# Kernel optimization log

Measured on AMD Instinct MI355X. Metric: run time of the kernel, lower is better.

Reference implementation:

```python
import jax, jax.numpy as jnp
import numpy as np

N_NODES = 100000


def gcn_conv(x, src, dst, deg_inv_sqrt, W, b):
    # x: [N, Fin], src/dst: [E_total] (self-loops included), W: [Fin, Fout]
    h = x @ W                                  # [N, Fout]
    norm = deg_inv_sqrt[src] * deg_inv_sqrt[dst]  # [E_total]
    msgs = h[src] * norm[:, None]              # [E_total, Fout] gather
    out = jax.ops.segment_sum(msgs, dst, num_segments=N_NODES)  # scatter-add
    return out + b


def setup_inputs() -> dict:
    key = jax.random.key(0)
    k1, k2, k3, k4, k5, k6, k7, k8 = jax.random.split(key, 8)
    input_dim, hidden_dim, out_dim = 4, 64, 2
    n_edges = 3200000
    x = jax.random.normal(k1, (N_NODES, input_dim), dtype=jnp.float32)
    edge_index = jax.random.randint(k2, (2, n_edges), 0, N_NODES, dtype=jnp.int64)
    s1 = 1.0 / np.sqrt(input_dim)
    s2 = 1.0 / np.sqrt(hidden_dim)
    W1 = jax.random.uniform(k3, (input_dim, hidden_dim), jnp.float32, -s1, s1)
    b1 = jnp.zeros((hidden_dim,), jnp.float32)
    W2 = jax.random.uniform(k4, (hidden_dim, hidden_dim), jnp.float32, -s2, s2)
    b2 = jnp.zeros((hidden_dim,), jnp.float32)
    Wf = jax.random.uniform(k5, (hidden_dim, out_dim), jnp.float32, -s2, s2)
    bf = jax.random.uniform(k6, (out_dim,), jnp.float32, -s2, s2)
    return {"x": x, "edge_index": edge_index, "W1": W1, "b1": b1,
            "W2": W2, "b2": b2, "Wf": Wf, "bf": bf}


def reference(x, edge_index, W1, b1, W2, b2, Wf, bf):
    # Add self-loops (PyG GCNConv default)
    loop = jnp.arange(N_NODES, dtype=edge_index.dtype)
    src = jnp.concatenate([edge_index[0], loop])
    dst = jnp.concatenate([edge_index[1], loop])
    # Symmetric normalization: degree on destination after self-loops
    deg = jax.ops.segment_sum(jnp.ones_like(dst, dtype=x.dtype), dst,
                              num_segments=N_NODES)
    deg_inv_sqrt = jnp.where(deg > 0, jax.lax.rsqrt(deg), 0.0)
    h = jax.nn.relu(gcn_conv(x, src, dst, deg_inv_sqrt, W1, b1))
    h = jax.nn.relu(gcn_conv(h, src, dst, deg_inv_sqrt, W2, b2))
    return h @ Wf + bf
```

## Files before the change

### kernel.cpp

```cpp
#include <hip/hip_runtime.h>
#include <hip/hip_bf16.h>

#define N_NODES 100000
#define N_EDGES 3200000
#define NB ((N_NODES + 255) / 256)
#define NBUCKET NB
#define EPB 8192
#define NPB ((N_EDGES + EPB - 1) / EPB)
#define BCAP 11264
#define KF_TILES (N_NODES / 16)
#define KF_BLOCKS ((KF_TILES + 3) / 4)
#define GCS 16
#define AGG_Q 4
#define AGG_QN (N_NODES / AGG_Q)

typedef short short8 __attribute__((ext_vector_type(8)));
typedef float f32x4 __attribute__((ext_vector_type(4)));

__device__ inline unsigned f2bf(float f) {
  unsigned x = __float_as_uint(f);
  return (x + 0x7FFFu + ((x >> 16) & 1u)) >> 16;
}


__global__ void __launch_bounds__(256) k_pass1(const int* __restrict__ src,
                                               const int* __restrict__ dst,
                                               int* __restrict__ gcur,
                                               unsigned int* __restrict__ eb) {
  __shared__ int hist[NBUCKET];
  __shared__ int gbase[NBUCKET];
  int tid = threadIdx.x;
  int base = blockIdx.x * EPB;
  int cnt = min(EPB, N_EDGES - base);
  int n4 = cnt >> 2;
  for (int i = tid; i < NBUCKET; i += 256) hist[i] = 0;
  __syncthreads();
  const int4* d4 = (const int4*)(dst + base);
  const int4* s4 = (const int4*)(src + base);
  unsigned mv[32];
  unsigned short mb[32];
#pragma unroll
  for (int k = 0; k < 8; ++k) {
    int i = tid + (k << 8);
    if (i < n4) {
      int4 dv = d4[i];
      int4 sv = s4[i];
      int b0 = dv.x >> 8, b1_ = dv.y >> 8, b2 = dv.z >> 8, b3 = dv.w >> 8;
      unsigned p0 = atomicAdd(&hist[b0], 1);
      unsigned p1 = atomicAdd(&hist[b1_], 1);
      unsigned p2 = atomicAdd(&hist[b2], 1);
      unsigned p3 = atomicAdd(&hist[b3], 1);
      mv[4 * k + 0] = (unsigned)sv.x | ((unsigned)(dv.x & 255) << 17) | (p0 << 25);
      mv[4 * k + 1] = (unsigned)sv.y | ((unsigned)(dv.y & 255) << 17) | (p1 << 25);
      mv[4 * k + 2] = (unsigned)sv.z | ((unsigned)(dv.z & 255) << 17) | (p2 << 25);
      mv[4 * k + 3] = (unsigned)sv.w | ((unsigned)(dv.w & 255) << 17) | (p3 << 25);
      mb[4 * k + 0] = (unsigned short)b0;
      mb[4 * k + 1] = (unsigned short)b1_;
      mb[4 * k + 2] = (unsigned short)b2;
      mb[4 * k + 3] = (unsigned short)b3;
    } else {
      mb[4 * k + 0] = 0xFFFF; mb[4 * k + 1] = 0xFFFF;
      mb[4 * k + 2] = 0xFFFF; mb[4 * k + 3] = 0xFFFF;
    }
  }
  __syncthreads();
  for (int b = tid; b < NBUCKET; b += 256) {
    int h = hist[b];
    gbase[b] = h ? atomicAdd(&gcur[b * GCS], h) : 0;
  }
  __syncthreads();
#pragma unroll
  for (int k = 0; k < 32; ++k) {
    if (mb[k] != 0xFFFF) {
      int b = mb[k];
      unsigned v = mv[k];
      unsigned pos = (unsigned)gbase[b] + (v >> 25);
      if (pos < BCAP) eb[(size_t)b * BCAP + pos] = v & 0x01FFFFFFu;
    }
  }
}


__global__ void __launch_bounds__(256) k_part2(unsigned int* __restrict__ eb,
                                               const int* __restrict__ gcur,
                                               int* __restrict__ rs, int* __restrict__ re,
                                               float* __restrict__ dis,
                                               const float4* __restrict__ x4,
                                               float4* __restrict__ xd) {
  __shared__ int hist[256], scn[256], cur[256];
  __shared__ int wsum[4];
  __shared__ int tot;
  __shared__ unsigned int stage[BCAP];
  int b = blockIdx.x, tid = threadIdx.x;
  int lane = tid & 63, wid = tid >> 6;
  int n0 = b << 8;
  int cnt = gcur[b * GCS];
  int base = b * BCAP;
  hist[tid] = 0; cur[tid] = 0;
  __syncthreads();
  for (int i = tid; i < cnt; i += 256)
    atomicAdd(&hist[eb[base + i] >> 17], 1);
  __syncthreads();
  int n = n0 + tid;
  int deg = hist[tid];
  int slots = (n < N_NODES) ? ((deg + 1 + 7) & ~7) : 0;
  int v = slots;
#pragma unroll
  for (int off = 1; off < 64; off <<= 1) {
    int t = __shfl_up(v, off);
    if (lane >= off) v += t;
  }
  if (lane == 63) wsum[wid] = v;
  __syncthreads();
  int x = v;
#pragma unroll
  for (int w2 = 0; w2 < 3; ++w2)
    if (wid > w2) x += wsum[w2];
  int excl = x - slots;
  if (tid == 255) tot = x;
  if (n < N_NODES) {
    rs[n]  = base + excl;
    re[n]  = base + excl + deg + 1;
    float dn = rsqrtf((float)(deg + 1));
    dis[n] = dn;
    float4 xv = x4[n];
    float4 w; w.x = xv.x * dn; w.y = xv.y * dn; w.z = xv.z * dn; w.w = xv.w * dn;
    xd[n] = w;
    stage[excl] = (unsigned)n;
    for (int i = deg + 1; i < slots; ++i)
      stage[excl + i] = (unsigned)N_NODES;
  }
  if (b == 0 && tid == 0) xd[N_NODES] = make_float4(0.f, 0.f, 0.f, 0.f);
  scn[tid] = excl + 1;
  __syncthreads();
  for (int i = tid; i < cnt; i += 256) {
    unsigned v2 = eb[base + i];
    unsigned low = v2 >> 17;
    int lpos = scn[low] + atomicAdd(&cur[low], 1);
    stage[lpos] = v2 & 0x1FFFFu;
  }
  __syncthreads();
  int total = tot;
  for (int i = tid; i < total; i += 256)
    eb[base + i] = stage[i];
  if (tid < 16) {
    int gp = total + tid;
    if (gp < BCAP) eb[base + gp] = (unsigned)N_NODES;
  }
}


__global__ void __launch_bounds__(256) k_l1(const float4* __restrict__ xd,
                                            const float* __restrict__ dis,
                                            const int* __restrict__ rs,
                                            const int* __restrict__ re,
                                            const int* __restrict__ csr,
                                            const float* __restrict__ W1,
                                            const float* __restrict__ b1,
                                            unsigned int* __restrict__ h1o) {
  int gt = blockIdx.x * 256 + threadIdx.x;
  int nid = gt >> 2, p = gt & 3;
  if (nid > N_NODES) return;
  if (nid == N_NODES) {
    uint4 z = make_uint4(0u, 0u, 0u, 0u);
    uint4* op = (uint4*)(h1o + nid * 32 + p * 8);
    op[0] = z; op[1] = z;
    return;
  }
  int e0 = rs[nid];
  int it4 = ((re[nid] - e0 + 7) & ~7) >> 2;
  const int* cp = csr + e0 + p;
  float ax = 0.f, ay = 0.f, az = 0.f, aw = 0.f;
#pragma unroll 4
  for (int t = 0; t < it4; ++t) {
    int s = cp[t << 2];
    float4 v = xd[s];
    ax += v.x; ay += v.y; az += v.z; aw += v.w;
  }
  ax += __shfl_xor(ax, 1); ax += __shfl_xor(ax, 2);
  ay += __shfl_xor(ay, 1); ay += __shfl_xor(ay, 2);
  az += __shfl_xor(az, 1); az += __shfl_xor(az, 2);
  aw += __shfl_xor(aw, 1); aw += __shfl_xor(aw, 2);
  float dn = dis[nid];
  ax *= dn; ay *= dn; az *= dn; aw *= dn;
  int j0 = p << 4;
  unsigned ou[8];
#pragma unroll
  for (int j2 = 0; j2 < 8; ++j2) {
    int j = j0 + j2 * 2;
    float s0 = b1[j]     + ax * W1[j]     + ay * W1[64 + j]     + az * W1[128 + j]     + aw * W1[192 + j];
    float s1 = b1[j + 1] + ax * W1[j + 1] + ay * W1[64 + j + 1] + az * W1[128 + j + 1] + aw * W1[192 + j + 1];
    unsigned u0 = f2bf(fmaxf(s0, 0.f) * dn);
    unsigned u1 = f2bf(fmaxf(s1, 0.f) * dn);
    ou[j2] = u0 | (u1 << 16);
  }
  uint4* op = (uint4*)(h1o + nid * 32 + p * 8);
  op[0] = make_uint4(ou[0], ou[1], ou[2], ou[3]);
  op[1] = make_uint4(ou[4], ou[5], ou[6], ou[7]);
}


__device__ inline void acc_bf2(float& a0, float& a1, unsigned u) {
  a0 += __uint_as_float(u << 16);
  a1 += __uint_as_float(u & 0xffff0000u);
}

__global__ void __launch_bounds__(256)
k_agg(const __hip_bfloat16* __restrict__ h1s, const float* __restrict__ dis,
      const int* __restrict__ rs, const int* __restrict__ re,
      const int* __restrict__ csr, unsigned short* __restrict__ aggb,
      int n_base) {
  int l = threadIdx.x & 63;
  int w = threadIdx.x >> 6;
  int n = n_base + blockIdx.x * 4 + w;
  int g = l >> 3;
  int c = l & 7;

  const unsigned int* h32 = (const unsigned int*)h1s;
  int e0 = rs[n];
  int iter = (re[n] - e0 + 7) >> 3;
  const int* cb = csr + e0 + g;
  int coff = c << 2;

  float a0 = 0.f, a1 = 0.f, a2 = 0.f, a3 = 0.f;
  float a4 = 0.f, a5 = 0.f, a6 = 0.f, a7 = 0.f;
  int sc = cb[0];
  int sn = cb[8];
  uint4 u = *(const uint4*)(h32 + (sc << 5) + coff);
  for (int it = 1; it < iter; ++it) {
    int sf = cb[(it + 1) << 3];
    uint4 r = *(const uint4*)(h32 + (sn << 5) + coff);
    acc_bf2(a0, a1, u.x); acc_bf2(a2, a3, u.y);
    acc_bf2(a4, a5, u.z); acc_bf2(a6, a7, u.w);
    u = r; sn = sf;
  }
  acc_bf2(a0, a1, u.x); acc_bf2(a2, a3, u.y);
  acc_bf2(a4, a5, u.z); acc_bf2(a6, a7, u.w);

#define RED3(a) a += __shfl_xor(a, 8); a += __shfl_xor(a, 16); a += __shfl_xor(a, 32);
  RED3(a0) RED3(a1) RED3(a2) RED3(a3) RED3(a4) RED3(a5) RED3(a6) RED3(a7)
#undef RED3

  float dn = dis[n];
  if (l < 8) {
    unsigned q0 = f2bf(a0 * dn) | (f2bf(a1 * dn) << 16);
    unsigned q1 = f2bf(a2 * dn) | (f2bf(a3 * dn) << 16);
    unsigned q2 = f2bf(a4 * dn) | (f2bf(a5 * dn) << 16);
    unsigned q3 = f2bf(a6 * dn) | (f2bf(a7 * dn) << 16);
    uint4* ap = (uint4*)(aggb + (size_t)n * 64 + (l << 3));
    *ap = make_uint4(q0, q1, q2, q3);
  }
}


__global__ void __launch_bounds__(256)
k_final(const unsigned short* __restrict__ aggb, const float* __restrict__ W2,
        const float* __restrict__ b2, const float* __restrict__ Wf,
        const float* __restrict__ bf, float* __restrict__ out) {
  int lane = threadIdx.x & 63;
  int wv = (blockIdx.x << 2) + (threadIdx.x >> 6);
  if (wv >= KF_TILES) return;
  int n0 = wv << 4;
  int m = lane & 15;
  int kg = lane >> 4;

  short8 bfr[2][4];
#pragma unroll
  for (int kt = 0; kt < 2; ++kt) {
#pragma unroll
    for (int nt = 0; nt < 4; ++nt) {
      short8 t;
#pragma unroll
      for (int j = 0; j < 8; ++j) {
        int k = kt * 32 + kg * 8 + j;
        t[j] = (short)f2bf(W2[k * 64 + nt * 16 + m]);
      }
      bfr[kt][nt] = t;
    }
  }
  const unsigned short* ar = aggb + (size_t)(n0 + m) * 64 + kg * 8;
  short8 a0 = *(const short8*)(ar);
  short8 a1 = *(const short8*)(ar + 32);

  f32x4 z = {0.f, 0.f, 0.f, 0.f};
  f32x4 acc0 = z, acc1 = z, acc2 = z, acc3 = z;
  acc0 = __builtin_amdgcn_mfma_f32_16x16x32_bf16(a0, bfr[0][0], acc0, 0, 0, 0);
  acc1 = __builtin_amdgcn_mfma_f32_16x16x32_bf16(a0, bfr[0][1], acc1, 0, 0, 0);
  acc2 = __builtin_amdgcn_mfma_f32_16x16x32_bf16(a0, bfr[0][2], acc2, 0, 0, 0);
  acc3 = __builtin_amdgcn_mfma_f32_16x16x32_bf16(a0, bfr[0][3], acc3, 0, 0, 0);
  acc0 = __builtin_amdgcn_mfma_f32_16x16x32_bf16(a1, bfr[1][0], acc0, 0, 0, 0);
  acc1 = __builtin_amdgcn_mfma_f32_16x16x32_bf16(a1, bfr[1][1], acc1, 0, 0, 0);
  acc2 = __builtin_amdgcn_mfma_f32_16x16x32_bf16(a1, bfr[1][2], acc2, 0, 0, 0);
  acc3 = __builtin_amdgcn_mfma_f32_16x16x32_bf16(a1, bfr[1][3], acc3, 0, 0, 0);

  float p0[4] = {0.f, 0.f, 0.f, 0.f};
  float p1[4] = {0.f, 0.f, 0.f, 0.f};
#pragma unroll
  for (int nt = 0; nt < 4; ++nt) {
    int col = nt * 16 + m;
    float bb = b2[col];
    float w0 = Wf[col * 2 + 0];
    float w1 = Wf[col * 2 + 1];
    f32x4 av = (nt == 0) ? acc0 : (nt == 1) ? acc1 : (nt == 2) ? acc2 : acc3;
#pragma unroll
    for (int r = 0; r < 4; ++r) {
      float tv = fmaxf(av[r] + bb, 0.f);
      p0[r] = fmaf(tv, w0, p0[r]);
      p1[r] = fmaf(tv, w1, p1[r]);
    }
  }
#pragma unroll
  for (int r = 0; r < 4; ++r) {
    p0[r] += __shfl_xor(p0[r], 1); p0[r] += __shfl_xor(p0[r], 2);
    p0[r] += __shfl_xor(p0[r], 4); p0[r] += __shfl_xor(p0[r], 8);
    p1[r] += __shfl_xor(p1[r], 1); p1[r] += __shfl_xor(p1[r], 2);
    p1[r] += __shfl_xor(p1[r], 4); p1[r] += __shfl_xor(p1[r], 8);
  }
  float bf0 = bf[0], bf1 = bf[1];
  int rowb = n0 + kg * 4;
  if (m == 0) *(float2*)(out + (rowb + 0) * 2) = make_float2(p0[0] + bf0, p1[0] + bf1);
  if (m == 1) *(float2*)(out + (rowb + 1) * 2) = make_float2(p0[1] + bf0, p1[1] + bf1);
  if (m == 2) *(float2*)(out + (rowb + 2) * 2) = make_float2(p0[2] + bf0, p1[2] + bf1);
  if (m == 3) *(float2*)(out + (rowb + 3) * 2) = make_float2(p0[3] + bf0, p1[3] + bf1);
}


extern "C" void kernel_launch(void* const* d_in, const int* in_sizes, int n_in,
                              void* d_out, int out_size, void* d_ws, size_t ws_size,
                              hipStream_t stream) {
  const float* x  = (const float*)d_in[0];
  const int*   ei = (const int*)d_in[1];
  const float* W1 = (const float*)d_in[2];
  const float* b1 = (const float*)d_in[3];
  const float* W2 = (const float*)d_in[4];
  const float* b2 = (const float*)d_in[5];
  const float* Wf = (const float*)d_in[6];
  const float* bf = (const float*)d_in[7];
  float* out = (float*)d_out;

  const int* srcv = ei;
  const int* dstv = ei + N_EDGES;

  char* p = (char*)d_ws;
  auto take = [&](size_t bytes) { char* r = p; p += (bytes + 255) & ~(size_t)255; return r; };
  int*          gcur = (int*)take((size_t)NBUCKET * GCS * 4);
  unsigned int* eb   = (unsigned int*)take((size_t)NBUCKET * BCAP * 4 + 512);
  int*          rs   = (int*)take((size_t)N_NODES * 4);
  int*          re   = (int*)take((size_t)N_NODES * 4);
  float*        dis  = (float*)take((size_t)N_NODES * 4);
  float4*       xd   = (float4*)take((size_t)(N_NODES + 1) * 16);
  __hip_bfloat16* h1s = (__hip_bfloat16*)take((size_t)(N_NODES + 1) * 64 * 2);
  unsigned short* aggb = (unsigned short*)take((size_t)N_NODES * 64 * 2);

  (void)hipMemsetAsync(gcur, 0, (size_t)NBUCKET * GCS * 4, stream);
  k_pass1<<<NPB, 256, 0, stream>>>(srcv, dstv, gcur, eb);
  k_part2<<<NBUCKET, 256, 0, stream>>>(eb, gcur, rs, re, dis, (const float4*)x, xd);
  const int* csr = (const int*)eb;
  k_l1<<<((N_NODES + 1) * 4 + 255) / 256, 256, 0, stream>>>(xd, dis, rs, re, csr, W1, b1, (unsigned int*)h1s);
  for (int q = 0; q < AGG_Q; ++q)
    k_agg<<<AGG_QN / 4, 256, 0, stream>>>(h1s, dis, rs, re, csr, aggb, q * AGG_QN);
  k_final<<<KF_BLOCKS, 256, 0, stream>>>(aggb, W2, b2, Wf, bf, out);
}
```

Before: 236.5 us.

## Fuse layer-2 aggregation with final MFMA projection via shared memory

Merges the aggregation kernel and the final dense kernel into one. Each 1024-thread block aggregates 16 nodes, one per wave, stages the bf16 rows in LDS, and wave 0 then runs the MFMA projection with bias, ReLU and the output layer. This drops the global round trip of the intermediate aggregation buffer and several kernel launches. In exchange, 15 of 16 waves sit idle during the projection and the block-wide barrier adds stalls. The larger blocks may also lower occupancy for the gather phase.

```diff
diff --git a/kernel.cpp b/kernel.cpp
--- a/kernel.cpp
+++ b/kernel.cpp
@@ -8,11 +8,7 @@
 #define EPB 8192
 #define NPB ((N_EDGES + EPB - 1) / EPB)
 #define BCAP 11264
-#define KF_TILES (N_NODES / 16)
-#define KF_BLOCKS ((KF_TILES + 3) / 4)
 #define GCS 16
-#define AGG_Q 4
-#define AGG_QN (N_NODES / AGG_Q)
 
 typedef short short8 __attribute__((ext_vector_type(8)));
 typedef float f32x4 __attribute__((ext_vector_type(4)));
@@ -205,14 +201,17 @@
   a1 += __uint_as_float(u & 0xffff0000u);
 }
 
-__global__ void __launch_bounds__(256)
+__global__ void __launch_bounds__(1024)
 k_agg(const __hip_bfloat16* __restrict__ h1s, const float* __restrict__ dis,
       const int* __restrict__ rs, const int* __restrict__ re,
-      const int* __restrict__ csr, unsigned short* __restrict__ aggb,
-      int n_base) {
+      const int* __restrict__ csr,
+      const float* __restrict__ W2, const float* __restrict__ b2,
+      const float* __restrict__ Wf, const float* __restrict__ bf,
+      float* __restrict__ out) {
+  __shared__ unsigned short arow[16][72];
   int l = threadIdx.x & 63;
-  int w = threadIdx.x >> 6;
-  int n = n_base + blockIdx.x * 4 + w;
+  int wid = threadIdx.x >> 6;
+  int n = blockIdx.x * 16 + wid;
   int g = l >> 3;
   int c = l & 7;
 
@@ -247,22 +246,14 @@
     unsigned q1 = f2bf(a2 * dn) | (f2bf(a3 * dn) << 16);
     unsigned q2 = f2bf(a4 * dn) | (f2bf(a5 * dn) << 16);
     unsigned q3 = f2bf(a6 * dn) | (f2bf(a7 * dn) << 16);
-    uint4* ap = (uint4*)(aggb + (size_t)n * 64 + (l << 3));
-    *ap = make_uint4(q0, q1, q2, q3);
-  }
-}
-
-
-__global__ void __launch_bounds__(256)
-k_final(const unsigned short* __restrict__ aggb, const float* __restrict__ W2,
-        const float* __restrict__ b2, const float* __restrict__ Wf,
-        const float* __restrict__ bf, float* __restrict__ out) {
-  int lane = threadIdx.x & 63;
-  int wv = (blockIdx.x << 2) + (threadIdx.x >> 6);
-  if (wv >= KF_TILES) return;
-  int n0 = wv << 4;
-  int m = lane & 15;
-  int kg = lane >> 4;
+    *(uint4*)&arow[wid][l << 3] = make_uint4(q0, q1, q2, q3);
+  }
+  __syncthreads();
+  if (wid != 0) return;
+
+  int n0 = blockIdx.x * 16;
+  int m = l & 15;
+  int kg = l >> 4;
 
   short8 bfr[2][4];
 #pragma unroll
@@ -278,20 +269,20 @@
       bfr[kt][nt] = t;
     }
   }
-  const unsigned short* ar = aggb + (size_t)(n0 + m) * 64 + kg * 8;
-  short8 a0 = *(const short8*)(ar);
-  short8 a1 = *(const short8*)(ar + 32);
+  const unsigned short* ar = &arow[m][kg << 3];
+  short8 af0 = *(const short8*)(ar);
+  short8 af1 = *(const short8*)(ar + 32);
 
   f32x4 z = {0.f, 0.f, 0.f, 0.f};
   f32x4 acc0 = z, acc1 = z, acc2 = z, acc3 = z;
-  acc0 = __builtin_amdgcn_mfma_f32_16x16x32_bf16(a0, bfr[0][0], acc0, 0, 0, 0);
-  acc1 = __builtin_amdgcn_mfma_f32_16x16x32_bf16(a0, bfr[0][1], acc1, 0, 0, 0);
-  acc2 = __builtin_amdgcn_mfma_f32_16x16x32_bf16(a0, bfr[0][2], acc2, 0, 0, 0);
-  acc3 = __builtin_amdgcn_mfma_f32_16x16x32_bf16(a0, bfr[0][3], acc3, 0, 0, 0);
-  acc0 = __builtin_amdgcn_mfma_f32_16x16x32_bf16(a1, bfr[1][0], acc0, 0, 0, 0);
-  acc1 = __builtin_amdgcn_mfma_f32_16x16x32_bf16(a1, bfr[1][1], acc1, 0, 0, 0);
-  acc2 = __builtin_amdgcn_mfma_f32_16x16x32_bf16(a1, bfr[1][2], acc2, 0, 0, 0);
-  acc3 = __builtin_amdgcn_mfma_f32_16x16x32_bf16(a1, bfr[1][3], acc3, 0, 0, 0);
+  acc0 = __builtin_amdgcn_mfma_f32_16x16x32_bf16(af0, bfr[0][0], acc0, 0, 0, 0);
+  acc1 = __builtin_amdgcn_mfma_f32_16x16x32_bf16(af0, bfr[0][1], acc1, 0, 0, 0);
+  acc2 = __builtin_amdgcn_mfma_f32_16x16x32_bf16(af0, bfr[0][2], acc2, 0, 0, 0);
+  acc3 = __builtin_amdgcn_mfma_f32_16x16x32_bf16(af0, bfr[0][3], acc3, 0, 0, 0);
+  acc0 = __builtin_amdgcn_mfma_f32_16x16x32_bf16(af1, bfr[1][0], acc0, 0, 0, 0);
+  acc1 = __builtin_amdgcn_mfma_f32_16x16x32_bf16(af1, bfr[1][1], acc1, 0, 0, 0);
+  acc2 = __builtin_amdgcn_mfma_f32_16x16x32_bf16(af1, bfr[1][2], acc2, 0, 0, 0);
+  acc3 = __builtin_amdgcn_mfma_f32_16x16x32_bf16(af1, bfr[1][3], acc3, 0, 0, 0);
 
   float p0[4] = {0.f, 0.f, 0.f, 0.f};
   float p1[4] = {0.f, 0.f, 0.f, 0.f};
@@ -350,14 +341,11 @@
   float*        dis  = (float*)take((size_t)N_NODES * 4);
   float4*       xd   = (float4*)take((size_t)(N_NODES + 1) * 16);
   __hip_bfloat16* h1s = (__hip_bfloat16*)take((size_t)(N_NODES + 1) * 64 * 2);
-  unsigned short* aggb = (unsigned short*)take((size_t)N_NODES * 64 * 2);
 
   (void)hipMemsetAsync(gcur, 0, (size_t)NBUCKET * GCS * 4, stream);
   k_pass1<<<NPB, 256, 0, stream>>>(srcv, dstv, gcur, eb);
   k_part2<<<NBUCKET, 256, 0, stream>>>(eb, gcur, rs, re, dis, (const float4*)x, xd);
   const int* csr = (const int*)eb;
   k_l1<<<((N_NODES + 1) * 4 + 255) / 256, 256, 0, stream>>>(xd, dis, rs, re, csr, W1, b1, (unsigned int*)h1s);
-  for (int q = 0; q < AGG_Q; ++q)
-    k_agg<<<AGG_QN / 4, 256, 0, stream>>>(h1s, dis, rs, re, csr, aggb, q * AGG_QN);
-  k_final<<<KF_BLOCKS, 256, 0, stream>>>(aggb, W2, b2, Wf, bf, out);
-}
+  k_agg<<<N_NODES / 16, 1024, 0, stream>>>(h1s, dis, rs, re, csr, W2, b2, Wf, bf, out);
+}
```

Result: slower. 248.0 us (+4.9%).
